# Kernel optimization log

Hardware: AMD Instinct MI355X
Metric: run time of the kernel (lower is better)

## Reference

```python
import jax, jax.numpy as jnp
import numpy as np

N, NQ, M, DQ, DK, DV, H = 4, 512, 512, 256, 256, 256, 256


def setup_inputs() -> dict:
    key = jax.random.key(0)
    ks = jax.random.split(key, 6)
    scale_q = 1.0 / np.sqrt(DQ)
    scale_k = 1.0 / np.sqrt(DK)
    scale_v = 1.0 / np.sqrt(H)
    return {
        "query": jax.random.normal(ks[0], (N, NQ, DQ), jnp.float32),
        "key": jax.random.normal(ks[1], (N, M, DK), jnp.float32),
        "value": jax.random.normal(ks[2], (N, M, DV), jnp.float32),
        "W_q": jax.random.normal(ks[3], (DQ, H), jnp.float32) * scale_q,
        "W_k": jax.random.normal(ks[4], (DK, H), jnp.float32) * scale_k,
        "W_v": jax.random.normal(ks[5], (H,), jnp.float32) * scale_v,
    }


def reference(query, key, value, W_q, W_k, W_v):
    # project: (N, n, H) and (N, m, H)
    q = jnp.einsum("bnd,dh->bnh", query, W_q)
    k = jnp.einsum("bmd,dh->bmh", key, W_k)
    # broadcast add -> (N, n, m, H), tanh, project H->1 -> scores (N, n, m)
    scores = jnp.einsum("bnmh,h->bnm", jnp.tanh(q[:, :, None, :] + k[:, None, :, :]), W_v)
    attn = jax.nn.softmax(scores, axis=-1)  # (N, n, m)
    return jnp.einsum("bnm,bmv->bnv", attn, value)
```

## Files before the change

kernel.cpp:

```cpp
#include <hip/hip_runtime.h>
#include <hip/hip_bf16.h>

#define NB 4
#define NQL 512
#define ML 512
#define DDIM 256
#define HDIM 256

static constexpr float TWO_LOG2E = 2.8853900817779268f;
static constexpr float LOG2E     = 1.4426950408889634f;

__global__ __launch_bounds__(256) void proj_kernel(
    const float* __restrict__ q_src, const float* __restrict__ k_src,
    const float* __restrict__ Wq,    const float* __restrict__ Wk,
    float* __restrict__ EqT,         float* __restrict__ EkT)
{
    const int z = blockIdx.z;
    const int b = z & 3;
    const int which = z >> 2;
    const float* __restrict__ src  = which ? k_src : q_src;
    const float* __restrict__ W    = which ? Wk    : Wq;
    float* __restrict__       outT = which ? EkT   : EqT;

    const int l0 = blockIdx.x * 32;
    const int h0 = blockIdx.y * 64;
    const int t  = threadIdx.x;
    const int tx = t & 15;
    const int ty = t >> 4;

    __shared__ float sX[32][36];
    __shared__ float sW[32][68];

    float acc[2][4];
    #pragma unroll
    for (int i = 0; i < 2; i++)
        #pragma unroll
        for (int j = 0; j < 4; j++) acc[i][j] = 0.f;

    const int llA = t >> 3, dgA = t & 7;
    const int ddB = t >> 3, hgB = t & 7;

    for (int d0 = 0; d0 < DDIM; d0 += 32) {
        float4 xv = *(const float4*)&src[(size_t)(b * NQL + l0 + llA) * DDIM + d0 + dgA * 4];
        const float* wrow = &W[(size_t)(d0 + ddB) * HDIM + h0 + hgB * 8];
        float4 wa = ((const float4*)wrow)[0];
        float4 wb = ((const float4*)wrow)[1];
        __syncthreads();
        sX[dgA * 4 + 0][llA] = xv.x;
        sX[dgA * 4 + 1][llA] = xv.y;
        sX[dgA * 4 + 2][llA] = xv.z;
        sX[dgA * 4 + 3][llA] = xv.w;
        *(float4*)&sW[ddB][hgB * 8]     = wa;
        *(float4*)&sW[ddB][hgB * 8 + 4] = wb;
        __syncthreads();
        #pragma unroll
        for (int dd = 0; dd < 32; dd++) {
            float4 w4 = *(const float4*)&sW[dd][tx * 4];
            float2 x2 = *(const float2*)&sX[dd][ty * 2];
            acc[0][0] = fmaf(x2.x, w4.x, acc[0][0]);
            acc[0][1] = fmaf(x2.x, w4.y, acc[0][1]);
            acc[0][2] = fmaf(x2.x, w4.z, acc[0][2]);
            acc[0][3] = fmaf(x2.x, w4.w, acc[0][3]);
            acc[1][0] = fmaf(x2.y, w4.x, acc[1][0]);
            acc[1][1] = fmaf(x2.y, w4.y, acc[1][1]);
            acc[1][2] = fmaf(x2.y, w4.z, acc[1][2]);
            acc[1][3] = fmaf(x2.y, w4.w, acc[1][3]);
        }
    }

    #pragma unroll
    for (int j = 0; j < 4; j++) {
        float2 o;
        o.x = __builtin_amdgcn_exp2f(acc[0][j] * TWO_LOG2E);
        o.y = __builtin_amdgcn_exp2f(acc[1][j] * TWO_LOG2E);
        *(float2*)&outT[(size_t)(b * HDIM + h0 + tx * 4 + j) * NQL + l0 + ty * 2] = o;
    }
}

__global__ __launch_bounds__(256) void scores_kernel(
    const float* __restrict__ EqT, const float* __restrict__ EkT,
    const float* __restrict__ Wv, float* __restrict__ S)
{
    const int b  = blockIdx.z;
    const int m0 = blockIdx.x * 32;
    const int n0 = blockIdx.y * 32;
    const int t  = threadIdx.x;
    const int tx = t & 15;
    const int ty = t >> 4;

    __shared__ float sQ[32][36];
    __shared__ float sK[32][36];
    __shared__ float sWV[32];

    float acc00 = 0.f, acc01 = 0.f, acc10 = 0.f, acc11 = 0.f;
    float swv = 0.f;

    const int hhA = t >> 3, cgA = t & 7;

    for (int h0 = 0; h0 < HDIM; h0 += 32) {
        float4 qv = *(const float4*)&EqT[(size_t)(b * HDIM + h0 + hhA) * NQL + n0 + cgA * 4];
        float4 kv = *(const float4*)&EkT[(size_t)(b * HDIM + h0 + hhA) * ML  + m0 + cgA * 4];
        float wv_ld = (t < 32) ? Wv[h0 + t] : 0.f;
        __syncthreads();
        *(float4*)&sQ[hhA][cgA * 4] = qv;
        *(float4*)&sK[hhA][cgA * 4] = kv;
        if (t < 32) sWV[t] = wv_ld;
        __syncthreads();
        #pragma unroll 8
        for (int hh = 0; hh < 32; hh++) {
            float2 q2 = *(const float2*)&sQ[hh][ty * 2];
            float2 k2 = *(const float2*)&sK[hh][tx * 2];
            float wv = sWV[hh];
            swv += wv;
            const float nw2 = -2.0f * wv;
            float a00 = fmaf(q2.x, k2.x, 1.0f);
            float a01 = fmaf(q2.x, k2.y, 1.0f);
            float a10 = fmaf(q2.y, k2.x, 1.0f);
            float a11 = fmaf(q2.y, k2.y, 1.0f);
            float r0 = __builtin_amdgcn_rcpf(a00 * a01);
            float r1 = __builtin_amdgcn_rcpf(a10 * a11);
            acc00 = fmaf(nw2, r0 * a01, acc00);
            acc01 = fmaf(nw2, r0 * a00, acc01);
            acc10 = fmaf(nw2, r1 * a11, acc10);
            acc11 = fmaf(nw2, r1 * a10, acc11);
        }
    }

    float2 o0 = {swv + acc00, swv + acc01};
    float2 o1 = {swv + acc10, swv + acc11};
    *(float2*)&S[(size_t)(b * NQL + n0 + ty * 2 + 0) * ML + m0 + tx * 2] = o0;
    *(float2*)&S[(size_t)(b * NQL + n0 + ty * 2 + 1) * ML + m0 + tx * 2] = o1;
}

__global__ __launch_bounds__(256) void softmax_kernel(float* __restrict__ S)
{
    const int row = blockIdx.x;
    float* p = &S[(size_t)row * ML];
    const int t = threadIdx.x;
    const int lane = t & 63, wid = t >> 6;

    float a = p[t];
    float c = p[t + 256];
    float mx = fmaxf(a, c);
    #pragma unroll
    for (int off = 32; off > 0; off >>= 1)
        mx = fmaxf(mx, __shfl_down(mx, off, 64));

    __shared__ float red[8];
    if (lane == 0) red[wid] = mx;
    __syncthreads();
    mx = fmaxf(fmaxf(red[0], red[1]), fmaxf(red[2], red[3]));

    float e0 = __builtin_amdgcn_exp2f((a - mx) * LOG2E);
    float e1 = __builtin_amdgcn_exp2f((c - mx) * LOG2E);
    float s = e0 + e1;
    #pragma unroll
    for (int off = 32; off > 0; off >>= 1)
        s += __shfl_down(s, off, 64);
    if (lane == 0) red[4 + wid] = s;
    __syncthreads();
    const float tot = red[4] + red[5] + red[6] + red[7];
    const float inv = 1.0f / tot;
    p[t]       = e0 * inv;
    p[t + 256] = e1 * inv;
}

__global__ __launch_bounds__(256) void av_kernel(
    const float* __restrict__ A, const float* __restrict__ V,
    float* __restrict__ O)
{
    const int b  = blockIdx.z;
    const int v0 = blockIdx.x * 64;
    const int n0 = blockIdx.y * 16;
    const int t  = threadIdx.x;
    const int tx = t & 15;
    const int ty = t >> 4;

    __shared__ float sA[32][20];
    __shared__ float sV[32][68];

    float4 acc = {0.f, 0.f, 0.f, 0.f};

    const int nnA = t >> 4, mgA = t & 15;
    const int mmB = t >> 3, vgB = t & 7;

    for (int m0 = 0; m0 < ML; m0 += 32) {
        float2 av = *(const float2*)&A[(size_t)(b * NQL + n0 + nnA) * ML + m0 + mgA * 2];
        const float* vrow = &V[(size_t)(b * ML + m0 + mmB) * DDIM + v0 + vgB * 8];
        float4 va = ((const float4*)vrow)[0];
        float4 vb = ((const float4*)vrow)[1];
        __syncthreads();
        sA[mgA * 2 + 0][nnA] = av.x;
        sA[mgA * 2 + 1][nnA] = av.y;
        *(float4*)&sV[mmB][vgB * 8]     = va;
        *(float4*)&sV[mmB][vgB * 8 + 4] = vb;
        __syncthreads();
        #pragma unroll
        for (int mm = 0; mm < 32; mm++) {
            float a = sA[mm][ty];
            float4 v4 = *(const float4*)&sV[mm][tx * 4];
            acc.x = fmaf(a, v4.x, acc.x);
            acc.y = fmaf(a, v4.y, acc.y);
            acc.z = fmaf(a, v4.z, acc.z);
            acc.w = fmaf(a, v4.w, acc.w);
        }
    }

    *(float4*)&O[(size_t)(b * NQL + n0 + ty) * DDIM + v0 + tx * 4] = acc;
}

extern "C" void kernel_launch(void* const* d_in, const int* in_sizes, int n_in,
                              void* d_out, int out_size, void* d_ws, size_t ws_size,
                              hipStream_t stream)
{
    const float* query = (const float*)d_in[0];
    const float* key   = (const float*)d_in[1];
    const float* value = (const float*)d_in[2];
    const float* Wq    = (const float*)d_in[3];
    const float* Wk    = (const float*)d_in[4];
    const float* Wv    = (const float*)d_in[5];
    float* out = (float*)d_out;

    float* EqT = (float*)d_ws;
    float* EkT = EqT + (size_t)NB * HDIM * NQL;
    float* S   = EkT + (size_t)NB * HDIM * ML;

    dim3 gProj(NQL / 32, HDIM / 64, NB * 2);
    proj_kernel<<<gProj, 256, 0, stream>>>(query, key, Wq, Wk, EqT, EkT);

    dim3 gSc(ML / 32, NQL / 32, NB);
    scores_kernel<<<gSc, 256, 0, stream>>>(EqT, EkT, Wv, S);

    softmax_kernel<<<dim3(NB * NQL), 256, 0, stream>>>(S);

    dim3 gAv(DDIM / 64, NQL / 16, NB);
    av_kernel<<<gAv, 256, 0, stream>>>(S, value, out);
}
```

Baseline: 133.7 us.

## Fuse softmax into scores/AV kernels, enlarge register tiles, add register prefetch

Removes the separate softmax kernel. The scores kernel now writes exp(score) together with partial row sums for each 64-column tile, and the AV kernel sums those partials and normalises its output by the inverse. The proj, scores and AV kernels get larger per-thread register tiles (4x4) and load the next tile into registers before the current one is computed. The AV kernel now uses 128 threads, splits m across two waves and combines them in LDS. Skipping the max subtraction risks overflow if scores grow large; here the tanh-bounded scores keep it safe.

```diff
diff --git a/kernel.cpp b/kernel.cpp
--- a/kernel.cpp
+++ b/kernel.cpp
@@ -1,5 +1,4 @@
 #include <hip/hip_runtime.h>
-#include <hip/hip_bf16.h>
 
 #define NB 4
 #define NQL 512
@@ -22,191 +21,290 @@
     const float* __restrict__ W    = which ? Wk    : Wq;
     float* __restrict__       outT = which ? EkT   : EqT;
 
-    const int l0 = blockIdx.x * 32;
+    const int l0 = blockIdx.x * 64;
     const int h0 = blockIdx.y * 64;
     const int t  = threadIdx.x;
     const int tx = t & 15;
     const int ty = t >> 4;
 
-    __shared__ float sX[32][36];
+    __shared__ float sX[64][36];
     __shared__ float sW[32][68];
 
-    float acc[2][4];
-    #pragma unroll
-    for (int i = 0; i < 2; i++)
+    const int rA = t >> 2, cgA = t & 3;
+    const int rB = t >> 3, cgB = t & 7;
+
+    float acc[4][4];
+    #pragma unroll
+    for (int i = 0; i < 4; i++)
         #pragma unroll
         for (int j = 0; j < 4; j++) acc[i][j] = 0.f;
 
-    const int llA = t >> 3, dgA = t & 7;
-    const int ddB = t >> 3, hgB = t & 7;
+    const float* xp0 = &src[(size_t)(b * NQL + l0 + rA) * DDIM + cgA * 8];
+    float4 xa = ((const float4*)xp0)[0];
+    float4 xb = ((const float4*)xp0)[1];
+    const float* wp0 = &W[(size_t)rB * HDIM + h0 + cgB * 8];
+    float4 wa = ((const float4*)wp0)[0];
+    float4 wb = ((const float4*)wp0)[1];
 
     for (int d0 = 0; d0 < DDIM; d0 += 32) {
-        float4 xv = *(const float4*)&src[(size_t)(b * NQL + l0 + llA) * DDIM + d0 + dgA * 4];
-        const float* wrow = &W[(size_t)(d0 + ddB) * HDIM + h0 + hgB * 8];
-        float4 wa = ((const float4*)wrow)[0];
-        float4 wb = ((const float4*)wrow)[1];
-        __syncthreads();
-        sX[dgA * 4 + 0][llA] = xv.x;
-        sX[dgA * 4 + 1][llA] = xv.y;
-        sX[dgA * 4 + 2][llA] = xv.z;
-        sX[dgA * 4 + 3][llA] = xv.w;
-        *(float4*)&sW[ddB][hgB * 8]     = wa;
-        *(float4*)&sW[ddB][hgB * 8 + 4] = wb;
-        __syncthreads();
-        #pragma unroll
-        for (int dd = 0; dd < 32; dd++) {
-            float4 w4 = *(const float4*)&sW[dd][tx * 4];
-            float2 x2 = *(const float2*)&sX[dd][ty * 2];
-            acc[0][0] = fmaf(x2.x, w4.x, acc[0][0]);
-            acc[0][1] = fmaf(x2.x, w4.y, acc[0][1]);
-            acc[0][2] = fmaf(x2.x, w4.z, acc[0][2]);
-            acc[0][3] = fmaf(x2.x, w4.w, acc[0][3]);
-            acc[1][0] = fmaf(x2.y, w4.x, acc[1][0]);
-            acc[1][1] = fmaf(x2.y, w4.y, acc[1][1]);
-            acc[1][2] = fmaf(x2.y, w4.z, acc[1][2]);
-            acc[1][3] = fmaf(x2.y, w4.w, acc[1][3]);
+        __syncthreads();
+        *(float4*)&sX[rA][cgA * 8]     = xa;
+        *(float4*)&sX[rA][cgA * 8 + 4] = xb;
+        *(float4*)&sW[rB][cgB * 8]     = wa;
+        *(float4*)&sW[rB][cgB * 8 + 4] = wb;
+        __syncthreads();
+        if (d0 + 32 < DDIM) {
+            const float* xp = &src[(size_t)(b * NQL + l0 + rA) * DDIM + (d0 + 32) + cgA * 8];
+            xa = ((const float4*)xp)[0];
+            xb = ((const float4*)xp)[1];
+            const float* wp = &W[(size_t)(d0 + 32 + rB) * HDIM + h0 + cgB * 8];
+            wa = ((const float4*)wp)[0];
+            wb = ((const float4*)wp)[1];
+        }
+        #pragma unroll
+        for (int dc = 0; dc < 8; dc++) {
+            float4 w0 = *(const float4*)&sW[dc * 4 + 0][tx * 4];
+            float4 w1 = *(const float4*)&sW[dc * 4 + 1][tx * 4];
+            float4 w2 = *(const float4*)&sW[dc * 4 + 2][tx * 4];
+            float4 w3 = *(const float4*)&sW[dc * 4 + 3][tx * 4];
+            #pragma unroll
+            for (int i = 0; i < 4; i++) {
+                float4 x = *(const float4*)&sX[ty * 4 + i][dc * 4];
+                acc[i][0] = fmaf(x.x, w0.x, acc[i][0]);
+                acc[i][1] = fmaf(x.x, w0.y, acc[i][1]);
+                acc[i][2] = fmaf(x.x, w0.z, acc[i][2]);
+                acc[i][3] = fmaf(x.x, w0.w, acc[i][3]);
+                acc[i][0] = fmaf(x.y, w1.x, acc[i][0]);
+                acc[i][1] = fmaf(x.y, w1.y, acc[i][1]);
+                acc[i][2] = fmaf(x.y, w1.z, acc[i][2]);
+                acc[i][3] = fmaf(x.y, w1.w, acc[i][3]);
+                acc[i][0] = fmaf(x.z, w2.x, acc[i][0]);
+                acc[i][1] = fmaf(x.z, w2.y, acc[i][1]);
+                acc[i][2] = fmaf(x.z, w2.z, acc[i][2]);
+                acc[i][3] = fmaf(x.z, w2.w, acc[i][3]);
+                acc[i][0] = fmaf(x.w, w3.x, acc[i][0]);
+                acc[i][1] = fmaf(x.w, w3.y, acc[i][1]);
+                acc[i][2] = fmaf(x.w, w3.z, acc[i][2]);
+                acc[i][3] = fmaf(x.w, w3.w, acc[i][3]);
+            }
         }
     }
 
     #pragma unroll
     for (int j = 0; j < 4; j++) {
-        float2 o;
+        float4 o;
         o.x = __builtin_amdgcn_exp2f(acc[0][j] * TWO_LOG2E);
         o.y = __builtin_amdgcn_exp2f(acc[1][j] * TWO_LOG2E);
-        *(float2*)&outT[(size_t)(b * HDIM + h0 + tx * 4 + j) * NQL + l0 + ty * 2] = o;
+        o.z = __builtin_amdgcn_exp2f(acc[2][j] * TWO_LOG2E);
+        o.w = __builtin_amdgcn_exp2f(acc[3][j] * TWO_LOG2E);
+        *(float4*)&outT[(size_t)(b * HDIM + h0 + tx * 4 + j) * NQL + l0 + ty * 4] = o;
     }
 }
 
 __global__ __launch_bounds__(256) void scores_kernel(
     const float* __restrict__ EqT, const float* __restrict__ EkT,
-    const float* __restrict__ Wv, float* __restrict__ S)
+    const float* __restrict__ Wv, float* __restrict__ S,
+    float* __restrict__ Spart)
 {
     const int b  = blockIdx.z;
-    const int m0 = blockIdx.x * 32;
-    const int n0 = blockIdx.y * 32;
+    const int mt = blockIdx.x;
+    const int m0 = mt * 64;
+    const int n0 = blockIdx.y * 64;
     const int t  = threadIdx.x;
     const int tx = t & 15;
     const int ty = t >> 4;
 
-    __shared__ float sQ[32][36];
-    __shared__ float sK[32][36];
+    __shared__ float sQ[32][68];
+    __shared__ float sK[32][68];
     __shared__ float sWV[32];
 
-    float acc00 = 0.f, acc01 = 0.f, acc10 = 0.f, acc11 = 0.f;
+    const int rS = t >> 3, cgS = t & 7;
+
+    float acc[4][4];
+    #pragma unroll
+    for (int i = 0; i < 4; i++)
+        #pragma unroll
+        for (int j = 0; j < 4; j++) acc[i][j] = 0.f;
     float swv = 0.f;
 
-    const int hhA = t >> 3, cgA = t & 7;
+    const float* qp0 = &EqT[(size_t)(b * HDIM + rS) * NQL + n0 + cgS * 8];
+    float4 qa = ((const float4*)qp0)[0];
+    float4 qb = ((const float4*)qp0)[1];
+    const float* kp0 = &EkT[(size_t)(b * HDIM + rS) * ML + m0 + cgS * 8];
+    float4 ka = ((const float4*)kp0)[0];
+    float4 kb = ((const float4*)kp0)[1];
+    float wvp = (t < 32) ? Wv[t] : 0.f;
 
     for (int h0 = 0; h0 < HDIM; h0 += 32) {
-        float4 qv = *(const float4*)&EqT[(size_t)(b * HDIM + h0 + hhA) * NQL + n0 + cgA * 4];
-        float4 kv = *(const float4*)&EkT[(size_t)(b * HDIM + h0 + hhA) * ML  + m0 + cgA * 4];
-        float wv_ld = (t < 32) ? Wv[h0 + t] : 0.f;
-        __syncthreads();
-        *(float4*)&sQ[hhA][cgA * 4] = qv;
-        *(float4*)&sK[hhA][cgA * 4] = kv;
-        if (t < 32) sWV[t] = wv_ld;
-        __syncthreads();
-        #pragma unroll 8
+        __syncthreads();
+        *(float4*)&sQ[rS][cgS * 8]     = qa;
+        *(float4*)&sQ[rS][cgS * 8 + 4] = qb;
+        *(float4*)&sK[rS][cgS * 8]     = ka;
+        *(float4*)&sK[rS][cgS * 8 + 4] = kb;
+        if (t < 32) sWV[t] = wvp;
+        __syncthreads();
+        if (h0 + 32 < HDIM) {
+            const float* qp = &EqT[(size_t)(b * HDIM + h0 + 32 + rS) * NQL + n0 + cgS * 8];
+            qa = ((const float4*)qp)[0];
+            qb = ((const float4*)qp)[1];
+            const float* kp = &EkT[(size_t)(b * HDIM + h0 + 32 + rS) * ML + m0 + cgS * 8];
+            ka = ((const float4*)kp)[0];
+            kb = ((const float4*)kp)[1];
+            if (t < 32) wvp = Wv[h0 + 32 + t];
+        }
+        #pragma unroll
         for (int hh = 0; hh < 32; hh++) {
-            float2 q2 = *(const float2*)&sQ[hh][ty * 2];
-            float2 k2 = *(const float2*)&sK[hh][tx * 2];
+            float4 q4 = *(const float4*)&sQ[hh][ty * 4];
+            float4 k4 = *(const float4*)&sK[hh][tx * 4];
             float wv = sWV[hh];
             swv += wv;
             const float nw2 = -2.0f * wv;
-            float a00 = fmaf(q2.x, k2.x, 1.0f);
-            float a01 = fmaf(q2.x, k2.y, 1.0f);
-            float a10 = fmaf(q2.y, k2.x, 1.0f);
-            float a11 = fmaf(q2.y, k2.y, 1.0f);
-            float r0 = __builtin_amdgcn_rcpf(a00 * a01);
-            float r1 = __builtin_amdgcn_rcpf(a10 * a11);
-            acc00 = fmaf(nw2, r0 * a01, acc00);
-            acc01 = fmaf(nw2, r0 * a00, acc01);
-            acc10 = fmaf(nw2, r1 * a11, acc10);
-            acc11 = fmaf(nw2, r1 * a10, acc11);
-        }
-    }
-
-    float2 o0 = {swv + acc00, swv + acc01};
-    float2 o1 = {swv + acc10, swv + acc11};
-    *(float2*)&S[(size_t)(b * NQL + n0 + ty * 2 + 0) * ML + m0 + tx * 2] = o0;
-    *(float2*)&S[(size_t)(b * NQL + n0 + ty * 2 + 1) * ML + m0 + tx * 2] = o1;
+            float qv[4] = {q4.x, q4.y, q4.z, q4.w};
+            #pragma unroll
+            for (int i = 0; i < 4; i++) {
+                float a0 = fmaf(qv[i], k4.x, 1.0f);
+                float a1 = fmaf(qv[i], k4.y, 1.0f);
+                float a2 = fmaf(qv[i], k4.z, 1.0f);
+                float a3 = fmaf(qv[i], k4.w, 1.0f);
+                float r01 = __builtin_amdgcn_rcpf(a0 * a1);
+                float r23 = __builtin_amdgcn_rcpf(a2 * a3);
+                acc[i][0] = fmaf(nw2, r01 * a1, acc[i][0]);
+                acc[i][1] = fmaf(nw2, r01 * a0, acc[i][1]);
+                acc[i][2] = fmaf(nw2, r23 * a3, acc[i][2]);
+                acc[i][3] = fmaf(nw2, r23 * a2, acc[i][3]);
+            }
+        }
+    }
+
+    float rs[4];
+    #pragma unroll
+    for (int i = 0; i < 4; i++) {
+        float4 p;
+        p.x = __builtin_amdgcn_exp2f((swv + acc[i][0]) * LOG2E);
+        p.y = __builtin_amdgcn_exp2f((swv + acc[i][1]) * LOG2E);
+        p.z = __builtin_amdgcn_exp2f((swv + acc[i][2]) * LOG2E);
+        p.w = __builtin_amdgcn_exp2f((swv + acc[i][3]) * LOG2E);
+        *(float4*)&S[(size_t)(b * NQL + n0 + ty * 4 + i) * ML + m0 + tx * 4] = p;
+        rs[i] = (p.x + p.y) + (p.z + p.w);
+    }
+    #pragma unroll
+    for (int off = 1; off < 16; off <<= 1) {
+        #pragma unroll
+        for (int i = 0; i < 4; i++) rs[i] += __shfl_xor(rs[i], off);
+    }
+    if ((t & 15) == 0) {
+        #pragma unroll
+        for (int i = 0; i < 4; i++)
+            Spart[(size_t)(mt * NB + b) * NQL + n0 + ty * 4 + i] = rs[i];
+    }
 }
 
-__global__ __launch_bounds__(256) void softmax_kernel(float* __restrict__ S)
-{
-    const int row = blockIdx.x;
-    float* p = &S[(size_t)row * ML];
-    const int t = threadIdx.x;
-    const int lane = t & 63, wid = t >> 6;
-
-    float a = p[t];
-    float c = p[t + 256];
-    float mx = fmaxf(a, c);
-    #pragma unroll
-    for (int off = 32; off > 0; off >>= 1)
-        mx = fmaxf(mx, __shfl_down(mx, off, 64));
-
-    __shared__ float red[8];
-    if (lane == 0) red[wid] = mx;
-    __syncthreads();
-    mx = fmaxf(fmaxf(red[0], red[1]), fmaxf(red[2], red[3]));
-
-    float e0 = __builtin_amdgcn_exp2f((a - mx) * LOG2E);
-    float e1 = __builtin_amdgcn_exp2f((c - mx) * LOG2E);
-    float s = e0 + e1;
-    #pragma unroll
-    for (int off = 32; off > 0; off >>= 1)
-        s += __shfl_down(s, off, 64);
-    if (lane == 0) red[4 + wid] = s;
-    __syncthreads();
-    const float tot = red[4] + red[5] + red[6] + red[7];
-    const float inv = 1.0f / tot;
-    p[t]       = e0 * inv;
-    p[t + 256] = e1 * inv;
-}
-
-__global__ __launch_bounds__(256) void av_kernel(
-    const float* __restrict__ A, const float* __restrict__ V,
-    float* __restrict__ O)
+__global__ __launch_bounds__(128) void av_kernel(
+    const float* __restrict__ P, const float* __restrict__ Spart,
+    const float* __restrict__ V, float* __restrict__ O)
 {
     const int b  = blockIdx.z;
     const int v0 = blockIdx.x * 64;
     const int n0 = blockIdx.y * 16;
     const int t  = threadIdx.x;
-    const int tx = t & 15;
-    const int ty = t >> 4;
-
-    __shared__ float sA[32][20];
-    __shared__ float sV[32][68];
-
-    float4 acc = {0.f, 0.f, 0.f, 0.f};
-
-    const int nnA = t >> 4, mgA = t & 15;
-    const int mmB = t >> 3, vgB = t & 7;
-
-    for (int m0 = 0; m0 < ML; m0 += 32) {
-        float2 av = *(const float2*)&A[(size_t)(b * NQL + n0 + nnA) * ML + m0 + mgA * 2];
-        const float* vrow = &V[(size_t)(b * ML + m0 + mmB) * DDIM + v0 + vgB * 8];
-        float4 va = ((const float4*)vrow)[0];
-        float4 vb = ((const float4*)vrow)[1];
-        __syncthreads();
-        sA[mgA * 2 + 0][nnA] = av.x;
-        sA[mgA * 2 + 1][nnA] = av.y;
-        *(float4*)&sV[mmB][vgB * 8]     = va;
-        *(float4*)&sV[mmB][vgB * 8 + 4] = vb;
-        __syncthreads();
-        #pragma unroll
-        for (int mm = 0; mm < 32; mm++) {
-            float a = sA[mm][ty];
-            float4 v4 = *(const float4*)&sV[mm][tx * 4];
-            acc.x = fmaf(a, v4.x, acc.x);
-            acc.y = fmaf(a, v4.y, acc.y);
-            acc.z = fmaf(a, v4.z, acc.z);
-            acc.w = fmaf(a, v4.w, acc.w);
-        }
-    }
-
-    *(float4*)&O[(size_t)(b * NQL + n0 + ty) * DDIM + v0 + tx * 4] = acc;
+    const int lane = t & 63;
+    const int wid  = t >> 6;
+    const int tx = lane & 15;
+    const int tn = lane >> 4;
+
+    __shared__ float sV[64][68];
+    __shared__ float sInv[16];
+
+    if (t < 16) {
+        float s = 0.f;
+        #pragma unroll
+        for (int mt = 0; mt < 8; mt++)
+            s += Spart[(size_t)(mt * NB + b) * NQL + n0 + t];
+        sInv[t] = 1.0f / s;
+    }
+
+    float acc[4][4];
+    #pragma unroll
+    for (int i = 0; i < 4; i++)
+        #pragma unroll
+        for (int j = 0; j < 4; j++) acc[i][j] = 0.f;
+
+    const int rV = t >> 1, cgV = t & 1;
+    float4 p[8];
+    #pragma unroll
+    for (int k = 0; k < 8; k++)
+        p[k] = *(const float4*)&V[(size_t)(b * ML + rV) * DDIM + v0 + cgV * 32 + k * 4];
+
+    for (int m0 = 0; m0 < ML; m0 += 64) {
+        __syncthreads();
+        #pragma unroll
+        for (int k = 0; k < 8; k++)
+            *(float4*)&sV[rV][cgV * 32 + k * 4] = p[k];
+        __syncthreads();
+        if (m0 + 64 < ML) {
+            #pragma unroll
+            for (int k = 0; k < 8; k++)
+                p[k] = *(const float4*)&V[(size_t)(b * ML + m0 + 64 + rV) * DDIM + v0 + cgV * 32 + k * 4];
+        }
+        const int mb = wid * 32;
+        #pragma unroll
+        for (int mg = 0; mg < 8; mg++) {
+            float4 a0 = *(const float4*)&P[(size_t)(b * NQL + n0 + tn * 4 + 0) * ML + m0 + mb + mg * 4];
+            float4 a1 = *(const float4*)&P[(size_t)(b * NQL + n0 + tn * 4 + 1) * ML + m0 + mb + mg * 4];
+            float4 a2 = *(const float4*)&P[(size_t)(b * NQL + n0 + tn * 4 + 2) * ML + m0 + mb + mg * 4];
+            float4 a3 = *(const float4*)&P[(size_t)(b * NQL + n0 + tn * 4 + 3) * ML + m0 + mb + mg * 4];
+            float4 v0v = *(const float4*)&sV[mb + mg * 4 + 0][tx * 4];
+            float4 v1v = *(const float4*)&sV[mb + mg * 4 + 1][tx * 4];
+            float4 v2v = *(const float4*)&sV[mb + mg * 4 + 2][tx * 4];
+            float4 v3v = *(const float4*)&sV[mb + mg * 4 + 3][tx * 4];
+#define AV_ROW(i, a)                                                         \
+            acc[i][0] = fmaf(a.x, v0v.x, acc[i][0]);                         \
+            acc[i][1] = fmaf(a.x, v0v.y, acc[i][1]);                         \
+            acc[i][2] = fmaf(a.x, v0v.z, acc[i][2]);                         \
+            acc[i][3] = fmaf(a.x, v0v.w, acc[i][3]);                         \
+            acc[i][0] = fmaf(a.y, v1v.x, acc[i][0]);                         \
+            acc[i][1] = fmaf(a.y, v1v.y, acc[i][1]);                         \
+            acc[i][2] = fmaf(a.y, v1v.z, acc[i][2]);                         \
+            acc[i][3] = fmaf(a.y, v1v.w, acc[i][3]);                         \
+            acc[i][0] = fmaf(a.z, v2v.x, acc[i][0]);                         \
+            acc[i][1] = fmaf(a.z, v2v.y, acc[i][1]);                         \
+            acc[i][2] = fmaf(a.z, v2v.z, acc[i][2]);                         \
+            acc[i][3] = fmaf(a.z, v2v.w, acc[i][3]);                         \
+            acc[i][0] = fmaf(a.w, v3v.x, acc[i][0]);                         \
+            acc[i][1] = fmaf(a.w, v3v.y, acc[i][1]);                         \
+            acc[i][2] = fmaf(a.w, v3v.z, acc[i][2]);                         \
+            acc[i][3] = fmaf(a.w, v3v.w, acc[i][3]);
+            AV_ROW(0, a0)
+            AV_ROW(1, a1)
+            AV_ROW(2, a2)
+            AV_ROW(3, a3)
+#undef AV_ROW
+        }
+    }
+
+    __syncthreads();
+    float* sRed = &sV[0][0];
+    if (wid == 1) {
+        #pragma unroll
+        for (int i = 0; i < 4; i++) {
+            float4 r = {acc[i][0], acc[i][1], acc[i][2], acc[i][3]};
+            *(float4*)&sRed[(tn * 4 + i) * 64 + tx * 4] = r;
+        }
+    }
+    __syncthreads();
+    if (wid == 0) {
+        #pragma unroll
+        for (int i = 0; i < 4; i++) {
+            float4 r = *(const float4*)&sRed[(tn * 4 + i) * 64 + tx * 4];
+            float inv = sInv[tn * 4 + i];
+            float4 o;
+            o.x = (acc[i][0] + r.x) * inv;
+            o.y = (acc[i][1] + r.y) * inv;
+            o.z = (acc[i][2] + r.z) * inv;
+            o.w = (acc[i][3] + r.w) * inv;
+            *(float4*)&O[(size_t)(b * NQL + n0 + tn * 4 + i) * DDIM + v0 + tx * 4] = o;
+        }
+    }
 }
 
 extern "C" void kernel_launch(void* const* d_in, const int* in_sizes, int n_in,
@@ -221,18 +319,17 @@
     const float* Wv    = (const float*)d_in[5];
     float* out = (float*)d_out;
 
-    float* EqT = (float*)d_ws;
-    float* EkT = EqT + (size_t)NB * HDIM * NQL;
-    float* S   = EkT + (size_t)NB * HDIM * ML;
-
-    dim3 gProj(NQL / 32, HDIM / 64, NB * 2);
+    float* EqT   = (float*)d_ws;
+    float* EkT   = EqT + (size_t)NB * HDIM * NQL;
+    float* S     = EkT + (size_t)NB * HDIM * ML;
+    float* Spart = S + (size_t)NB * NQL * ML;
+
+    dim3 gProj(NQL / 64, HDIM / 64, NB * 2);
     proj_kernel<<<gProj, 256, 0, stream>>>(query, key, Wq, Wk, EqT, EkT);
 
-    dim3 gSc(ML / 32, NQL / 32, NB);
-    scores_kernel<<<gSc, 256, 0, stream>>>(EqT, EkT, Wv, S);
-
-    softmax_kernel<<<dim3(NB * NQL), 256, 0, stream>>>(S);
+    dim3 gSc(ML / 64, NQL / 64, NB);
+    scores_kernel<<<gSc, 256, 0, stream>>>(EqT, EkT, Wv, S, Spart);
 
     dim3 gAv(DDIM / 64, NQL / 16, NB);
-    av_kernel<<<gAv, 256, 0, stream>>>(S, value, out);
+    av_kernel<<<gAv, 128, 0, stream>>>(S, Spart, value, out);
 }
```

Result: slower. 151.9 us (+13.6%).

## Fuse softmax into scores and AV, drop LDS tiling for direct loads

Applied to the files above, without the earlier changes.

Removes the separate softmax kernel. The scores kernel now writes exp(score) without subtracting a max, plus per-row partial sums over four m-tiles. The AV kernel combines those partial sums and normalizes at the end. All kernels switch from shared-memory tiling to direct global float4 loads with larger per-thread tiles, and AV splits the M reduction across four waves reduced through LDS. Skipping the max subtraction relies on the scores being bounded, which holds here since |score| ≤ sum|Wv|.

```diff
diff --git a/kernel.cpp b/kernel.cpp
--- a/kernel.cpp
+++ b/kernel.cpp
@@ -1,5 +1,4 @@
 #include <hip/hip_runtime.h>
-#include <hip/hip_bf16.h>
 
 #define NB 4
 #define NQL 512
@@ -10,66 +9,55 @@
 static constexpr float TWO_LOG2E = 2.8853900817779268f;
 static constexpr float LOG2E     = 1.4426950408889634f;
 
-__global__ __launch_bounds__(256) void proj_kernel(
+__global__ __launch_bounds__(512) void proj_kernel(
     const float* __restrict__ q_src, const float* __restrict__ k_src,
     const float* __restrict__ Wq,    const float* __restrict__ Wk,
     float* __restrict__ EqT,         float* __restrict__ EkT)
 {
-    const int z = blockIdx.z;
-    const int b = z & 3;
-    const int which = z >> 2;
-    const float* __restrict__ src  = which ? k_src : q_src;
-    const float* __restrict__ W    = which ? Wk    : Wq;
-    float* __restrict__       outT = which ? EkT   : EqT;
-
-    const int l0 = blockIdx.x * 32;
-    const int h0 = blockIdx.y * 64;
+    const int idx   = blockIdx.x;
+    const int b     = idx & 3;
+    const int which = (idx >> 2) & 1;
+    const int lt    = (idx >> 3) & 7;
+    const int ht    = idx >> 6;
+    const float* __restrict__ src = which ? k_src : q_src;
+    const float* __restrict__ W   = which ? Wk : Wq;
+    float* __restrict__ outT      = which ? EkT : EqT;
+
+    const int l0 = lt * 64, h0 = ht * 64;
     const int t  = threadIdx.x;
     const int tx = t & 15;
     const int ty = t >> 4;
 
-    __shared__ float sX[32][36];
-    __shared__ float sW[32][68];
-
-    float acc[2][4];
+    const float* xp0 = &src[(size_t)(b * NQL + l0 + ty * 2) * DDIM];
+    const float* xp1 = xp0 + DDIM;
+    const float* wp  = &W[h0 + tx * 4];
+
+    float acc[2][4] = {{0.f, 0.f, 0.f, 0.f}, {0.f, 0.f, 0.f, 0.f}};
+
+    #pragma unroll 4
+    for (int dc = 0; dc < 64; ++dc) {
+        float4 xa = *(const float4*)(xp0 + dc * 4);
+        float4 xb = *(const float4*)(xp1 + dc * 4);
+        const float* wrow = wp + (size_t)dc * 4 * HDIM;
+        float4 w0 = *(const float4*)(wrow);
+        float4 w1 = *(const float4*)(wrow + HDIM);
+        float4 w2 = *(const float4*)(wrow + 2 * HDIM);
+        float4 w3 = *(const float4*)(wrow + 3 * HDIM);
+#define PJ(xv, wv)                                                   \
+        acc[0][0] = fmaf(xa.xv, wv.x, acc[0][0]);                    \
+        acc[0][1] = fmaf(xa.xv, wv.y, acc[0][1]);                    \
+        acc[0][2] = fmaf(xa.xv, wv.z, acc[0][2]);                    \
+        acc[0][3] = fmaf(xa.xv, wv.w, acc[0][3]);                    \
+        acc[1][0] = fmaf(xb.xv, wv.x, acc[1][0]);                    \
+        acc[1][1] = fmaf(xb.xv, wv.y, acc[1][1]);                    \
+        acc[1][2] = fmaf(xb.xv, wv.z, acc[1][2]);                    \
+        acc[1][3] = fmaf(xb.xv, wv.w, acc[1][3]);
+        PJ(x, w0) PJ(y, w1) PJ(z, w2) PJ(w, w3)
+#undef PJ
+    }
+
     #pragma unroll
-    for (int i = 0; i < 2; i++)
-        #pragma unroll
-        for (int j = 0; j < 4; j++) acc[i][j] = 0.f;
-
-    const int llA = t >> 3, dgA = t & 7;
-    const int ddB = t >> 3, hgB = t & 7;
-
-    for (int d0 = 0; d0 < DDIM; d0 += 32) {
-        float4 xv = *(const float4*)&src[(size_t)(b * NQL + l0 + llA) * DDIM + d0 + dgA * 4];
-        const float* wrow = &W[(size_t)(d0 + ddB) * HDIM + h0 + hgB * 8];
-        float4 wa = ((const float4*)wrow)[0];
-        float4 wb = ((const float4*)wrow)[1];
-        __syncthreads();
-        sX[dgA * 4 + 0][llA] = xv.x;
-        sX[dgA * 4 + 1][llA] = xv.y;
-        sX[dgA * 4 + 2][llA] = xv.z;
-        sX[dgA * 4 + 3][llA] = xv.w;
-        *(float4*)&sW[ddB][hgB * 8]     = wa;
-        *(float4*)&sW[ddB][hgB * 8 + 4] = wb;
-        __syncthreads();
-        #pragma unroll
-        for (int dd = 0; dd < 32; dd++) {
-            float4 w4 = *(const float4*)&sW[dd][tx * 4];
-            float2 x2 = *(const float2*)&sX[dd][ty * 2];
-            acc[0][0] = fmaf(x2.x, w4.x, acc[0][0]);
-            acc[0][1] = fmaf(x2.x, w4.y, acc[0][1]);
-            acc[0][2] = fmaf(x2.x, w4.z, acc[0][2]);
-            acc[0][3] = fmaf(x2.x, w4.w, acc[0][3]);
-            acc[1][0] = fmaf(x2.y, w4.x, acc[1][0]);
-            acc[1][1] = fmaf(x2.y, w4.y, acc[1][1]);
-            acc[1][2] = fmaf(x2.y, w4.z, acc[1][2]);
-            acc[1][3] = fmaf(x2.y, w4.w, acc[1][3]);
-        }
-    }
-
-    #pragma unroll
-    for (int j = 0; j < 4; j++) {
+    for (int j = 0; j < 4; ++j) {
         float2 o;
         o.x = __builtin_amdgcn_exp2f(acc[0][j] * TWO_LOG2E);
         o.y = __builtin_amdgcn_exp2f(acc[1][j] * TWO_LOG2E);
@@ -77,136 +65,178 @@
     }
 }
 
-__global__ __launch_bounds__(256) void scores_kernel(
+__global__ __launch_bounds__(512) void scores_kernel(
     const float* __restrict__ EqT, const float* __restrict__ EkT,
-    const float* __restrict__ Wv, float* __restrict__ S)
-{
-    const int b  = blockIdx.z;
-    const int m0 = blockIdx.x * 32;
-    const int n0 = blockIdx.y * 32;
-    const int t  = threadIdx.x;
-    const int tx = t & 15;
-    const int ty = t >> 4;
-
-    __shared__ float sQ[32][36];
-    __shared__ float sK[32][36];
-    __shared__ float sWV[32];
-
-    float acc00 = 0.f, acc01 = 0.f, acc10 = 0.f, acc11 = 0.f;
+    const float* __restrict__ Wv, float* __restrict__ P,
+    float* __restrict__ Spart)
+{
+    const int idx = blockIdx.x;
+    const int b   = idx & 3;
+    const int mt  = (idx >> 2) & 3;
+    const int nt  = idx >> 4;
+    const int m0  = mt * 128, n0 = nt * 32;
+    const int t   = threadIdx.x;
+    const int tx  = t & 31;
+    const int ty  = t >> 5;
+
+    const float* qp = &EqT[(size_t)b * HDIM * NQL + n0 + ty * 2];
+    const float* kp = &EkT[(size_t)b * HDIM * ML + m0 + tx * 4];
+
+    float acc0[4] = {0.f, 0.f, 0.f, 0.f};
+    float acc1[4] = {0.f, 0.f, 0.f, 0.f};
     float swv = 0.f;
 
-    const int hhA = t >> 3, cgA = t & 7;
-
-    for (int h0 = 0; h0 < HDIM; h0 += 32) {
-        float4 qv = *(const float4*)&EqT[(size_t)(b * HDIM + h0 + hhA) * NQL + n0 + cgA * 4];
-        float4 kv = *(const float4*)&EkT[(size_t)(b * HDIM + h0 + hhA) * ML  + m0 + cgA * 4];
-        float wv_ld = (t < 32) ? Wv[h0 + t] : 0.f;
-        __syncthreads();
-        *(float4*)&sQ[hhA][cgA * 4] = qv;
-        *(float4*)&sK[hhA][cgA * 4] = kv;
-        if (t < 32) sWV[t] = wv_ld;
-        __syncthreads();
-        #pragma unroll 8
-        for (int hh = 0; hh < 32; hh++) {
-            float2 q2 = *(const float2*)&sQ[hh][ty * 2];
-            float2 k2 = *(const float2*)&sK[hh][tx * 2];
-            float wv = sWV[hh];
-            swv += wv;
-            const float nw2 = -2.0f * wv;
-            float a00 = fmaf(q2.x, k2.x, 1.0f);
-            float a01 = fmaf(q2.x, k2.y, 1.0f);
-            float a10 = fmaf(q2.y, k2.x, 1.0f);
-            float a11 = fmaf(q2.y, k2.y, 1.0f);
-            float r0 = __builtin_amdgcn_rcpf(a00 * a01);
-            float r1 = __builtin_amdgcn_rcpf(a10 * a11);
-            acc00 = fmaf(nw2, r0 * a01, acc00);
-            acc01 = fmaf(nw2, r0 * a00, acc01);
-            acc10 = fmaf(nw2, r1 * a11, acc10);
-            acc11 = fmaf(nw2, r1 * a10, acc11);
-        }
-    }
-
-    float2 o0 = {swv + acc00, swv + acc01};
-    float2 o1 = {swv + acc10, swv + acc11};
-    *(float2*)&S[(size_t)(b * NQL + n0 + ty * 2 + 0) * ML + m0 + tx * 2] = o0;
-    *(float2*)&S[(size_t)(b * NQL + n0 + ty * 2 + 1) * ML + m0 + tx * 2] = o1;
-}
-
-__global__ __launch_bounds__(256) void softmax_kernel(float* __restrict__ S)
-{
-    const int row = blockIdx.x;
-    float* p = &S[(size_t)row * ML];
-    const int t = threadIdx.x;
-    const int lane = t & 63, wid = t >> 6;
-
-    float a = p[t];
-    float c = p[t + 256];
-    float mx = fmaxf(a, c);
+    #pragma unroll 4
+    for (int hh = 0; hh < HDIM; ++hh) {
+        float2 q2 = *(const float2*)(qp + (size_t)hh * NQL);
+        float4 k4 = *(const float4*)(kp + (size_t)hh * ML);
+        const float wv = Wv[hh];
+        swv += wv;
+        const float nw2 = -2.0f * wv;
+        {
+            float a0 = fmaf(q2.x, k4.x, 1.0f);
+            float a1 = fmaf(q2.x, k4.y, 1.0f);
+            float a2 = fmaf(q2.x, k4.z, 1.0f);
+            float a3 = fmaf(q2.x, k4.w, 1.0f);
+            float r01 = __builtin_amdgcn_rcpf(a0 * a1);
+            float r23 = __builtin_amdgcn_rcpf(a2 * a3);
+            acc0[0] = fmaf(nw2, r01 * a1, acc0[0]);
+            acc0[1] = fmaf(nw2, r01 * a0, acc0[1]);
+            acc0[2] = fmaf(nw2, r23 * a3, acc0[2]);
+            acc0[3] = fmaf(nw2, r23 * a2, acc0[3]);
+        }
+        {
+            float a0 = fmaf(q2.y, k4.x, 1.0f);
+            float a1 = fmaf(q2.y, k4.y, 1.0f);
+            float a2 = fmaf(q2.y, k4.z, 1.0f);
+            float a3 = fmaf(q2.y, k4.w, 1.0f);
+            float r01 = __builtin_amdgcn_rcpf(a0 * a1);
+            float r23 = __builtin_amdgcn_rcpf(a2 * a3);
+            acc1[0] = fmaf(nw2, r01 * a1, acc1[0]);
+            acc1[1] = fmaf(nw2, r01 * a0, acc1[1]);
+            acc1[2] = fmaf(nw2, r23 * a3, acc1[2]);
+            acc1[3] = fmaf(nw2, r23 * a2, acc1[3]);
+        }
+    }
+
+    float rs[2];
+    {
+        float4 p;
+        p.x = __builtin_amdgcn_exp2f((swv + acc0[0]) * LOG2E);
+        p.y = __builtin_amdgcn_exp2f((swv + acc0[1]) * LOG2E);
+        p.z = __builtin_amdgcn_exp2f((swv + acc0[2]) * LOG2E);
+        p.w = __builtin_amdgcn_exp2f((swv + acc0[3]) * LOG2E);
+        *(float4*)&P[(size_t)(b * NQL + n0 + ty * 2 + 0) * ML + m0 + tx * 4] = p;
+        rs[0] = (p.x + p.y) + (p.z + p.w);
+    }
+    {
+        float4 p;
+        p.x = __builtin_amdgcn_exp2f((swv + acc1[0]) * LOG2E);
+        p.y = __builtin_amdgcn_exp2f((swv + acc1[1]) * LOG2E);
+        p.z = __builtin_amdgcn_exp2f((swv + acc1[2]) * LOG2E);
+        p.w = __builtin_amdgcn_exp2f((swv + acc1[3]) * LOG2E);
+        *(float4*)&P[(size_t)(b * NQL + n0 + ty * 2 + 1) * ML + m0 + tx * 4] = p;
+        rs[1] = (p.x + p.y) + (p.z + p.w);
+    }
     #pragma unroll
-    for (int off = 32; off > 0; off >>= 1)
-        mx = fmaxf(mx, __shfl_down(mx, off, 64));
-
-    __shared__ float red[8];
-    if (lane == 0) red[wid] = mx;
+    for (int off = 1; off < 32; off <<= 1) {
+        rs[0] += __shfl_xor(rs[0], off);
+        rs[1] += __shfl_xor(rs[1], off);
+    }
+    if (tx == 0) {
+        float2 o = {rs[0], rs[1]};
+        *(float2*)&Spart[(size_t)(mt * NB + b) * NQL + n0 + ty * 2] = o;
+    }
+}
+
+__global__ __launch_bounds__(256) void av_kernel(
+    const float* __restrict__ P, const float* __restrict__ Spart,
+    const float* __restrict__ V, float* __restrict__ O)
+{
+    const int idx = blockIdx.x;
+    const int b   = idx & 3;
+    const int vt  = (idx >> 2) & 3;
+    const int nt  = idx >> 4;
+    const int v0  = vt * 64, n0 = nt * 16;
+    const int t    = threadIdx.x;
+    const int lane = t & 63;
+    const int wid  = t >> 6;
+    const int tx   = lane & 15;
+    const int tn   = lane >> 4;
+
+    __shared__ float sInv[16];
+    __shared__ float sRed[3][16][64];
+
+    if (t < 16) {
+        float s = 0.f;
+        #pragma unroll
+        for (int mt = 0; mt < 4; ++mt)
+            s += Spart[(size_t)(mt * NB + b) * NQL + n0 + t];
+        sInv[t] = 1.0f / s;
+    }
+
+    float acc[4][4] = {};
+    const int mbase = wid * 128;
+    const float* pbase = &P[(size_t)(b * NQL + n0 + tn * 4) * ML + mbase];
+    const float* vbase = &V[(size_t)(b * ML + mbase) * DDIM + v0 + tx * 4];
+
+    #pragma unroll 2
+    for (int mc = 0; mc < 32; ++mc) {
+        const float* pp = pbase + mc * 4;
+        float4 a0 = *(const float4*)(pp);
+        float4 a1 = *(const float4*)(pp + ML);
+        float4 a2 = *(const float4*)(pp + 2 * ML);
+        float4 a3 = *(const float4*)(pp + 3 * ML);
+        const float* vv = vbase + (size_t)mc * 4 * DDIM;
+        float4 vr0 = *(const float4*)(vv);
+        float4 vr1 = *(const float4*)(vv + DDIM);
+        float4 vr2 = *(const float4*)(vv + 2 * DDIM);
+        float4 vr3 = *(const float4*)(vv + 3 * DDIM);
+#define AVR(i, a)                                                    \
+        acc[i][0] = fmaf(a.x, vr0.x, acc[i][0]);                     \
+        acc[i][1] = fmaf(a.x, vr0.y, acc[i][1]);                     \
+        acc[i][2] = fmaf(a.x, vr0.z, acc[i][2]);                     \
+        acc[i][3] = fmaf(a.x, vr0.w, acc[i][3]);                     \
+        acc[i][0] = fmaf(a.y, vr1.x, acc[i][0]);                     \
+        acc[i][1] = fmaf(a.y, vr1.y, acc[i][1]);                     \
+        acc[i][2] = fmaf(a.y, vr1.z, acc[i][2]);                     \
+        acc[i][3] = fmaf(a.y, vr1.w, acc[i][3]);                     \
+        acc[i][0] = fmaf(a.z, vr2.x, acc[i][0]);                     \
+        acc[i][1] = fmaf(a.z, vr2.y, acc[i][1]);                     \
+        acc[i][2] = fmaf(a.z, vr2.z, acc[i][2]);                     \
+        acc[i][3] = fmaf(a.z, vr2.w, acc[i][3]);                     \
+        acc[i][0] = fmaf(a.w, vr3.x, acc[i][0]);                     \
+        acc[i][1] = fmaf(a.w, vr3.y, acc[i][1]);                     \
+        acc[i][2] = fmaf(a.w, vr3.z, acc[i][2]);                     \
+        acc[i][3] = fmaf(a.w, vr3.w, acc[i][3]);
+        AVR(0, a0) AVR(1, a1) AVR(2, a2) AVR(3, a3)
+#undef AVR
+    }
+
     __syncthreads();
-    mx = fmaxf(fmaxf(red[0], red[1]), fmaxf(red[2], red[3]));
-
-    float e0 = __builtin_amdgcn_exp2f((a - mx) * LOG2E);
-    float e1 = __builtin_amdgcn_exp2f((c - mx) * LOG2E);
-    float s = e0 + e1;
-    #pragma unroll
-    for (int off = 32; off > 0; off >>= 1)
-        s += __shfl_down(s, off, 64);
-    if (lane == 0) red[4 + wid] = s;
+    if (wid != 0) {
+        #pragma unroll
+        for (int i = 0; i < 4; ++i) {
+            float4 r = {acc[i][0], acc[i][1], acc[i][2], acc[i][3]};
+            *(float4*)&sRed[wid - 1][tn * 4 + i][tx * 4] = r;
+        }
+    }
     __syncthreads();
-    const float tot = red[4] + red[5] + red[6] + red[7];
-    const float inv = 1.0f / tot;
-    p[t]       = e0 * inv;
-    p[t + 256] = e1 * inv;
-}
-
-__global__ __launch_bounds__(256) void av_kernel(
-    const float* __restrict__ A, const float* __restrict__ V,
-    float* __restrict__ O)
-{
-    const int b  = blockIdx.z;
-    const int v0 = blockIdx.x * 64;
-    const int n0 = blockIdx.y * 16;
-    const int t  = threadIdx.x;
-    const int tx = t & 15;
-    const int ty = t >> 4;
-
-    __shared__ float sA[32][20];
-    __shared__ float sV[32][68];
-
-    float4 acc = {0.f, 0.f, 0.f, 0.f};
-
-    const int nnA = t >> 4, mgA = t & 15;
-    const int mmB = t >> 3, vgB = t & 7;
-
-    for (int m0 = 0; m0 < ML; m0 += 32) {
-        float2 av = *(const float2*)&A[(size_t)(b * NQL + n0 + nnA) * ML + m0 + mgA * 2];
-        const float* vrow = &V[(size_t)(b * ML + m0 + mmB) * DDIM + v0 + vgB * 8];
-        float4 va = ((const float4*)vrow)[0];
-        float4 vb = ((const float4*)vrow)[1];
-        __syncthreads();
-        sA[mgA * 2 + 0][nnA] = av.x;
-        sA[mgA * 2 + 1][nnA] = av.y;
-        *(float4*)&sV[mmB][vgB * 8]     = va;
-        *(float4*)&sV[mmB][vgB * 8 + 4] = vb;
-        __syncthreads();
+    if (wid == 0) {
         #pragma unroll
-        for (int mm = 0; mm < 32; mm++) {
-            float a = sA[mm][ty];
-            float4 v4 = *(const float4*)&sV[mm][tx * 4];
-            acc.x = fmaf(a, v4.x, acc.x);
-            acc.y = fmaf(a, v4.y, acc.y);
-            acc.z = fmaf(a, v4.z, acc.z);
-            acc.w = fmaf(a, v4.w, acc.w);
-        }
-    }
-
-    *(float4*)&O[(size_t)(b * NQL + n0 + ty) * DDIM + v0 + tx * 4] = acc;
+        for (int i = 0; i < 4; ++i) {
+            float4 r1 = *(const float4*)&sRed[0][tn * 4 + i][tx * 4];
+            float4 r2 = *(const float4*)&sRed[1][tn * 4 + i][tx * 4];
+            float4 r3 = *(const float4*)&sRed[2][tn * 4 + i][tx * 4];
+            const float inv = sInv[tn * 4 + i];
+            float4 o;
+            o.x = (acc[i][0] + r1.x + r2.x + r3.x) * inv;
+            o.y = (acc[i][1] + r1.y + r2.y + r3.y) * inv;
+            o.z = (acc[i][2] + r1.z + r2.z + r3.z) * inv;
+            o.w = (acc[i][3] + r1.w + r2.w + r3.w) * inv;
+            *(float4*)&O[(size_t)(b * NQL + n0 + tn * 4 + i) * DDIM + v0 + tx * 4] = o;
+        }
+    }
 }
 
 extern "C" void kernel_launch(void* const* d_in, const int* in_sizes, int n_in,
@@ -221,18 +251,12 @@
     const float* Wv    = (const float*)d_in[5];
     float* out = (float*)d_out;
 
-    float* EqT = (float*)d_ws;
-    float* EkT = EqT + (size_t)NB * HDIM * NQL;
-    float* S   = EkT + (size_t)NB * HDIM * ML;
-
-    dim3 gProj(NQL / 32, HDIM / 64, NB * 2);
-    proj_kernel<<<gProj, 256, 0, stream>>>(query, key, Wq, Wk, EqT, EkT);
-
-    dim3 gSc(ML / 32, NQL / 32, NB);
-    scores_kernel<<<gSc, 256, 0, stream>>>(EqT, EkT, Wv, S);
-
-    softmax_kernel<<<dim3(NB * NQL), 256, 0, stream>>>(S);
-
-    dim3 gAv(DDIM / 64, NQL / 16, NB);
-    av_kernel<<<gAv, 256, 0, stream>>>(S, value, out);
-}
+    float* EqT   = (float*)d_ws;
+    float* EkT   = EqT + (size_t)NB * HDIM * NQL;
+    float* P     = EkT + (size_t)NB * HDIM * ML;
+    float* Spart = P + (size_t)NB * NQL * ML;
+
+    proj_kernel<<<dim3(256), 512, 0, stream>>>(query, key, Wq, Wk, EqT, EkT);
+    scores_kernel<<<dim3(256), 512, 0, stream>>>(EqT, EkT, Wv, P, Spart);
+    av_kernel<<<dim3(512), 256, 0, stream>>>(P, Spart, value, out);
+}
```

Measured after the change: 146.8 us. 1.1x slower.
